# Kernel tuning notes

Measured on AMD Instinct MI355X. Metric: run time of the kernel, lower is better.

The kernel has to match this reference:

```python
import jax, jax.numpy as jnp
import numpy as np

WS = 7            # window size per spatial dim
NW = WS ** 3      # tokens per window = 343
EPS = 1e-5


def _rel_pos_index():
    # MONAI 3D relative position index, shape (NW, NW), values in [0, 13^3)
    coords = np.stack(np.meshgrid(np.arange(WS), np.arange(WS), np.arange(WS), indexing='ij'))
    cf = coords.reshape(3, -1)                       # (3, NW)
    rel = (cf[:, :, None] - cf[:, None, :]).transpose(1, 2, 0).astype(np.int64)  # (NW, NW, 3)
    rel += WS - 1
    rel[:, :, 0] *= (2 * WS - 1) * (2 * WS - 1)
    rel[:, :, 1] *= (2 * WS - 1)
    return rel.sum(-1)

_RPI = _rel_pos_index()


def layer_norm(x, g, b):
    mu = jnp.mean(x, axis=-1, keepdims=True)
    var = jnp.mean(jnp.square(x - mu), axis=-1, keepdims=True)
    return (x - mu) * jax.lax.rsqrt(var + EPS) * g + b


def _forward(x, pe_w, pe_bias, pe_g, pe_b, n1_g, n1_b, qkv_w, rpb, proj_w, proj_b,
             n2_g, n2_b, fc1_w, fc1_b, fc2_w, fc2_b):
    # ---- PatchEmbed: Conv3d stride=patch + LayerNorm over channel ----
    h = jax.lax.conv_general_dilated(x, pe_w, (2, 2, 2), 'VALID',
                                     dimension_numbers=('NCDHW', 'OIDHW', 'NCDHW'))
    h = h + pe_bias[None, :, None, None, None]
    b, c, d, hh, w = h.shape
    t = h.reshape(b, c, -1).transpose(0, 2, 1)       # (b, d*h*w, c)
    t = layer_norm(t, pe_g, pe_b)
    h = t.transpose(0, 2, 1).reshape(b, c, d, hh, w)
    # dropout(p=0) and proj_out(normalize=False) are identity

    xe = h.transpose(0, 2, 3, 4, 1)                  # (b, d, h, w, c)
    rpi = jnp.asarray(_RPI)
    num_heads = rpb.shape[-1]
    hd = c // num_heads
    scale = hd ** -0.5
    nd, nh_, nw_ = d // WS, hh // WS, w // WS        # window grid (7,7,7)

    for i in range(qkv_w.shape[0]):                  # 3 Swin blocks, all shift=0
        shortcut = xe
        y = layer_norm(xe, n1_g[i], n1_b[i])
        # window partition -> (b*nW, NW, c)
        yw = y.reshape(b, nd, WS, nh_, WS, nw_, WS, c)
        yw = yw.transpose(0, 1, 3, 5, 2, 4, 6, 7).reshape(-1, NW, c)
        # windowed MSA with relative position bias (qkv_bias=False)
        qkv = (yw @ qkv_w[i].T).reshape(-1, NW, 3, num_heads, hd).transpose(2, 0, 3, 1, 4)
        q, k, v = qkv[0] * scale, qkv[1], qkv[2]     # (Bw, nh, NW, hd)
        attn = jnp.einsum('bhnd,bhmd->bhnm', q, k)
        bias = rpb[i][rpi].transpose(2, 0, 1)        # (nh, NW, NW)
        attn = jax.nn.softmax(attn + bias[None], axis=-1)
        o = jnp.einsum('bhnm,bhmd->bhnd', attn, v)
        o = o.transpose(0, 2, 1, 3).reshape(-1, NW, c)
        o = o @ proj_w[i].T + proj_b[i]
        # window reverse
        o = o.reshape(b, nd, nh_, nw_, WS, WS, WS, c)
        o = o.transpose(0, 1, 4, 2, 5, 3, 6, 7).reshape(b, d, hh, w, c)
        xe = shortcut + o
        # MLP (GELU exact, mlp_ratio=4)
        z = layer_norm(xe, n2_g[i], n2_b[i])
        z = jax.nn.gelu(z @ fc1_w[i].T + fc1_b[i], approximate=False)
        xe = xe + (z @ fc2_w[i].T + fc2_b[i])

    return xe.transpose(0, 4, 1, 2, 3)               # (b, c, d, h, w)


def setup_inputs() -> dict:
    key = jax.random.key(0)
    ks = jax.random.split(key, 16)
    C, NH, NB, MLP = 16, 2, 3, 64
    s = 0.02
    return {
        'x': jax.random.normal(ks[0], (1, 1, 98, 98, 98), jnp.float32),
        'pe_w': jax.random.normal(ks[1], (C, 1, 2, 2, 2), jnp.float32) * s,
        'pe_bias': jnp.zeros((C,), jnp.float32),
        'pe_g': jnp.ones((C,), jnp.float32),
        'pe_b': jnp.zeros((C,), jnp.float32),
        'n1_g': jnp.ones((NB, C), jnp.float32),
        'n1_b': jnp.zeros((NB, C), jnp.float32),
        'qkv_w': jax.random.normal(ks[2], (NB, 3 * C, C), jnp.float32) * s,
        'rpb': jax.random.normal(ks[3], (NB, (2 * WS - 1) ** 3, NH), jnp.float32) * s,
        'proj_w': jax.random.normal(ks[4], (NB, C, C), jnp.float32) * s,
        'proj_b': jnp.zeros((NB, C), jnp.float32),
        'n2_g': jnp.ones((NB, C), jnp.float32),
        'n2_b': jnp.zeros((NB, C), jnp.float32),
        'fc1_w': jax.random.normal(ks[5], (NB, MLP, C), jnp.float32) * s,
        'fc1_b': jnp.zeros((NB, MLP), jnp.float32),
        'fc2_w': jax.random.normal(ks[6], (NB, C, MLP), jnp.float32) * s,
        'fc2_b': jnp.zeros((NB, C), jnp.float32),
    }


def reference(x, pe_w, pe_bias, pe_g, pe_b, n1_g, n1_b, qkv_w, rpb, proj_w, proj_b,
              n2_g, n2_b, fc1_w, fc1_b, fc2_w, fc2_b):
    return _forward(x, pe_w, pe_bias, pe_g, pe_b, n1_g, n1_b, qkv_w, rpb, proj_w,
                    proj_b, n2_g, n2_b, fc1_w, fc1_b, fc2_w, fc2_b)
```

## Files before the change

kernel.cpp:

```cpp
#include <hip/hip_runtime.h>
#include <math.h>

#define NWTOK 343
#define NTOK 117649
#define QSCALE 0.510069734f
#define LOG2E 1.4426950408889634f
#define QPLANE 1372
#define OPLANE 2744
#define NPAD 352
#define NTILE 22
#define NBIAS_BLK 2904
#define NK0_TILE 7546

typedef unsigned int u32;
typedef __fp16 h2 __attribute__((ext_vector_type(2)));
typedef __fp16 h4 __attribute__((ext_vector_type(4)));
typedef float f32x4 __attribute__((ext_vector_type(4)));

__device__ __forceinline__ u32 packh2(float a, float b) {
    h2 h = __builtin_amdgcn_cvt_pkrtz(a, b);
    return __builtin_bit_cast(u32, h);
}
__device__ __forceinline__ h4 packh4(float a, float b, float c, float d) {
    return __builtin_bit_cast(h4, make_uint2(packh2(a, b), packh2(c, d)));
}
__device__ __forceinline__ float fast_exp2(float x) {
#if __has_builtin(__builtin_amdgcn_exp2f)
    return __builtin_amdgcn_exp2f(x);
#else
    return exp2f(x);
#endif
}

__device__ __forceinline__ float gelu_exact(float x) {
    const float z = x * 0.70710678118654752f;
    const float az = fabsf(z);
    const float t = __builtin_amdgcn_rcpf(fmaf(0.3275911f, az, 1.0f));
    float y = fmaf(t, 1.061405429f, -1.453152027f);
    y = fmaf(t, y, 1.421413741f);
    y = fmaf(t, y, -0.284496736f);
    y = fmaf(t, y, 0.254829592f);
    y *= t;
    const float one_m_erf = y * __expf(-az * az);
    const float erf_az = 1.0f - one_m_erf;
    const float erf_z = (z < 0.f) ? -erf_az : erf_az;
    return 0.5f * x * (1.0f + erf_z);
}

__global__ __launch_bounds__(256, 4) void k0_fused(
    const float* __restrict__ x,
    const float* __restrict__ pe_w,
    const float* __restrict__ pe_bias,
    const float* __restrict__ pe_g,
    const float* __restrict__ pe_b,
    const float* __restrict__ n1_g,
    const float* __restrict__ n1_b,
    const float* __restrict__ qkv_w,
    const float* __restrict__ rpb,
    float* __restrict__ xe,
    u32* __restrict__ qg,
    u32* __restrict__ kg,
    u32* __restrict__ vg,
    __fp16* __restrict__ bexp16)
{
    const int tid = threadIdx.x;

    if (blockIdx.x < NBIAS_BLK) {
        const int tile = blockIdx.x;
        const int kt = tile % NTILE;
        const int rest = tile / NTILE;
        const int qt = rest % NTILE;
        const int bh = rest / NTILE;
        const int blk = bh >> 1, h = bh & 1;
        const int n = tid >> 4, g = tid & 15;
        const int i = qt * 16 + n, j = kt * 16 + g;
        float val;
        if (j >= NWTOK) {
            val = -60.f;
        } else if (i >= NWTOK) {
            val = 0.f;
        } else {
            const int iz = i / 49, ir = i - iz * 49, iy = ir / 7, ix = ir - iy * 7;
            const int jz = j / 49, jr = j - jz * 49, jy = jr / 7, jx = jr - jy * 7;
            const int idx = (iz - jz + 6) * 169 + (iy - jy + 6) * 13 + (ix - jx + 6);
            val = rpb[((size_t)blk * 2197 + idx) * 2 + h] * LOG2E;
        }
        bexp16[(size_t)tile * 256 + tid] = (__fp16)val;
        return;
    }

    __shared__ float pw_s[128];
    __shared__ u32 qkvh[384];
    __shared__ float pb_s[16], g_s[16], b_s[16], n1g_s[16], n1b_s[16];

    if (tid < 128) pw_s[tid] = pe_w[tid];
    for (int i = tid; i < 384; i += 256) {
        const float2 a = ((const float2*)qkv_w)[i];
        qkvh[i] = packh2(a.x, a.y);
    }
    if (tid < 16) {
        pb_s[tid] = pe_bias[tid]; g_s[tid] = pe_g[tid]; b_s[tid] = pe_b[tid];
        n1g_s[tid] = n1_g[tid]; n1b_s[tid] = n1_b[tid];
    }
    __syncthreads();

    const int wave_id = (blockIdx.x - NBIAS_BLK) * 4 + (tid >> 6);
    if (wave_id >= NK0_TILE) return;
    const int w = wave_id / NTILE;
    const int qt = wave_id - w * NTILE;

    const int lane = tid & 63;
    const int tcol = lane & 15;
    const int g4 = (lane >> 4) * 4;
    const int tok = qt * 16 + tcol;
    const bool valid = (tok < NWTOK);
    const int tokc = valid ? tok : (NWTOK - 1);

    const int wd = w / 49, wr = w - wd * 49, wh = wr / 7, ww = wr - wh * 7;
    const int tz = tokc / 49, tr = tokc - tz * 49, ty = tr / 7, tx = tr - ty * 7;
    const int z = wd * 7 + tz, y = wh * 7 + ty, xx = ww * 7 + tx;
    const float* bp = x + ((size_t)(2 * z) * 98 + (2 * y)) * 98 + 2 * xx;
    float in[8];
    in[0] = bp[0];    in[1] = bp[1];
    in[2] = bp[98];   in[3] = bp[99];
    in[4] = bp[9604]; in[5] = bp[9605];
    in[6] = bp[9702]; in[7] = bp[9703];

    float c4[4];
    #pragma unroll
    for (int i = 0; i < 4; ++i) {
        const int ch = g4 + i;
        const float4 w0 = *(const float4*)(pw_s + ch * 8);
        const float4 w1 = *(const float4*)(pw_s + ch * 8 + 4);
        float a = pb_s[ch];
        a = fmaf(in[0], w0.x, a); a = fmaf(in[1], w0.y, a);
        a = fmaf(in[2], w0.z, a); a = fmaf(in[3], w0.w, a);
        a = fmaf(in[4], w1.x, a); a = fmaf(in[5], w1.y, a);
        a = fmaf(in[6], w1.z, a); a = fmaf(in[7], w1.w, a);
        c4[i] = a;
    }

    float s = (c4[0] + c4[1]) + (c4[2] + c4[3]);
    s += __shfl_xor(s, 16); s += __shfl_xor(s, 32);
    float mu = s * 0.0625f;
    float v0 = c4[0] - mu, v1 = c4[1] - mu, v2 = c4[2] - mu, v3 = c4[3] - mu;
    float vv = fmaf(v0, v0, fmaf(v1, v1, fmaf(v2, v2, v3 * v3)));
    vv += __shfl_xor(vv, 16); vv += __shfl_xor(vv, 32);
    float rs = rsqrtf(vv * 0.0625f + 1e-5f);
    const float4 gg = *(const float4*)(g_s + g4);
    const float4 bb = *(const float4*)(b_s + g4);
    const float o0 = v0 * rs * gg.x + bb.x;
    const float o1 = v1 * rs * gg.y + bb.y;
    const float o2 = v2 * rs * gg.z + bb.z;
    const float o3 = v3 * rs * gg.w + bb.w;

    if (valid)
        *(float4*)(xe + (size_t)(w * NWTOK + tok) * 16 + g4) = make_float4(o0, o1, o2, o3);

    s = (o0 + o1) + (o2 + o3);
    s += __shfl_xor(s, 16); s += __shfl_xor(s, 32);
    mu = s * 0.0625f;
    v0 = o0 - mu; v1 = o1 - mu; v2 = o2 - mu; v3 = o3 - mu;
    vv = fmaf(v0, v0, fmaf(v1, v1, fmaf(v2, v2, v3 * v3)));
    vv += __shfl_xor(vv, 16); vv += __shfl_xor(vv, 32);
    rs = rsqrtf(vv * 0.0625f + 1e-5f);
    const float4 g1 = *(const float4*)(n1g_s + g4);
    const float4 b1 = *(const float4*)(n1b_s + g4);
    const h4 yB = packh4(v0 * rs * g1.x + b1.x, v1 * rs * g1.y + b1.y,
                         v2 * rs * g1.z + b1.z, v3 * rs * g1.w + b1.w);

    const f32x4 zero = {0.f, 0.f, 0.f, 0.f};
    const int head = g4 >> 3;
    const int uoff = (g4 & 7) >> 1;
    const size_t qpl = (size_t)(w * 2 + head) * QPLANE + tok * 4 + uoff;
    #pragma unroll
    for (int m = 0; m < 3; ++m) {
        const uint2 aw = *(const uint2*)(qkvh + (m * 16 + tcol) * 8 + (g4 >> 1));
        f32x4 d = __builtin_amdgcn_mfma_f32_16x16x16f16(
            __builtin_bit_cast(h4, aw), yB, zero, 0, 0, 0);
        const float sc = (m == 0) ? QSCALE : 1.f;
        const u32 lo = packh2(d[0] * sc, d[1] * sc);
        const u32 hi = packh2(d[2] * sc, d[3] * sc);
        if (valid) {
            u32* dst = (m == 0 ? qg : (m == 1 ? kg : vg)) + qpl;
            dst[0] = lo;
            dst[1] = hi;
        }
    }
}

__global__ __launch_bounds__(704, 5) void k_attn(
    const u32* __restrict__ qg,
    const u32* __restrict__ kg,
    const u32* __restrict__ vg,
    float* __restrict__ og,
    const __fp16* __restrict__ bexp_blk)
{
    __shared__ __fp16 Kl[2][NPAD][16];
    __shared__ __fp16 Ql[2][NPAD][16];
    __shared__ __fp16 Vt[2][16][360];

    const int tid = threadIdx.x;
    const int pidx = blockIdx.x;
    const int wp = pidx >> 1;
    const int h = pidx & 1;
    const int w0 = 2 * wp;
    const int w1 = (w0 + 1 < NWTOK) ? w0 + 1 : NWTOK - 1;
    const int wh0 = w0 * 2 + h;
    const int wh1 = w1 * 2 + h;

    {
        const int sw = (tid >= NPAD) ? 1 : 0;
        const int st = tid - sw * NPAD;
        const size_t qpl = (size_t)(sw ? wh1 : wh0) * QPLANE;
        const uint4 z4 = make_uint4(0, 0, 0, 0);
        if (st < NWTOK) {
            const uint4 kw = ((const uint4*)(kg + qpl))[st];
            const uint4 qw = ((const uint4*)(qg + qpl))[st];
            const uint4 vw = ((const uint4*)(vg + qpl))[st];
            *(uint4*)&Kl[sw][st][0] = kw; *(uint4*)&Kl[sw][st][8] = z4;
            *(uint4*)&Ql[sw][st][0] = qw; *(uint4*)&Ql[sw][st][8] = z4;
            const h2 v01 = __builtin_bit_cast(h2, vw.x);
            const h2 v23 = __builtin_bit_cast(h2, vw.y);
            const h2 v45 = __builtin_bit_cast(h2, vw.z);
            const h2 v67 = __builtin_bit_cast(h2, vw.w);
            Vt[sw][0][st] = v01.x; Vt[sw][1][st] = v01.y;
            Vt[sw][2][st] = v23.x; Vt[sw][3][st] = v23.y;
            Vt[sw][4][st] = v45.x; Vt[sw][5][st] = v45.y;
            Vt[sw][6][st] = v67.x; Vt[sw][7][st] = v67.y;
        } else {
            *(uint4*)&Kl[sw][st][0] = z4; *(uint4*)&Kl[sw][st][8] = z4;
            *(uint4*)&Ql[sw][st][0] = z4; *(uint4*)&Ql[sw][st][8] = z4;
            #pragma unroll
            for (int d = 0; d < 8; ++d) Vt[sw][d][st] = (__fp16)0.f;
        }
        #pragma unroll
        for (int d = 8; d < 16; ++d) Vt[sw][d][st] = (__fp16)0.f;
    }
    __syncthreads();

    const int wave = tid >> 6;
    const int lane = tid & 63;
    const int n = lane & 15;
    const int g4 = (lane >> 4) * 4;

    const int qiA = (2 * wave) * 16 + n;
    const int qiB = qiA + 16;
    const h4 bqA0 = *(const h4*)&Ql[0][qiA][g4];
    const h4 bqB0 = *(const h4*)&Ql[0][qiB][g4];
    const h4 bqA1 = *(const h4*)&Ql[1][qiA][g4];
    const h4 bqB1 = *(const h4*)&Ql[1][qiB][g4];

    const int laneoff = n * 16 + g4;
    const __fp16* trowA = bexp_blk + ((size_t)(h * 484) + (size_t)(2 * wave) * NTILE) * 256 + laneoff;
    const __fp16* trowB = trowA + (size_t)NTILE * 256;

    f32x4 accA0 = {0.f, 0.f, 0.f, 0.f}, accB0 = {0.f, 0.f, 0.f, 0.f};
    f32x4 accA1 = {0.f, 0.f, 0.f, 0.f}, accB1 = {0.f, 0.f, 0.f, 0.f};
    float lA0 = 0.f, lB0 = 0.f, lA1 = 0.f, lB1 = 0.f;

    #pragma unroll
    for (int kt = 0; kt < NTILE; ++kt) {
        const uint2 cbA16 = *(const uint2*)(trowA + kt * 256);
        const uint2 cbB16 = *(const uint2*)(trowB + kt * 256);
        const h2 alo = __builtin_bit_cast(h2, cbA16.x);
        const h2 ahi = __builtin_bit_cast(h2, cbA16.y);
        const h2 blo = __builtin_bit_cast(h2, cbB16.x);
        const h2 bhi = __builtin_bit_cast(h2, cbB16.y);
        f32x4 cbAf, cbBf;
        cbAf[0] = (float)alo.x; cbAf[1] = (float)alo.y;
        cbAf[2] = (float)ahi.x; cbAf[3] = (float)ahi.y;
        cbBf[0] = (float)blo.x; cbBf[1] = (float)blo.y;
        cbBf[2] = (float)bhi.x; cbBf[3] = (float)bhi.y;

        const h4 ak0 = *(const h4*)&Kl[0][kt * 16 + n][g4];
        const h4 ak1 = *(const h4*)&Kl[1][kt * 16 + n][g4];
        const h4 av0 = *(const h4*)&Vt[0][n][kt * 16 + g4];
        const h4 av1 = *(const h4*)&Vt[1][n][kt * 16 + g4];

        f32x4 sA0 = __builtin_amdgcn_mfma_f32_16x16x16f16(ak0, bqA0, cbAf, 0, 0, 0);
        f32x4 sB0 = __builtin_amdgcn_mfma_f32_16x16x16f16(ak0, bqB0, cbBf, 0, 0, 0);
        f32x4 sA1 = __builtin_amdgcn_mfma_f32_16x16x16f16(ak1, bqA1, cbAf, 0, 0, 0);
        f32x4 sB1 = __builtin_amdgcn_mfma_f32_16x16x16f16(ak1, bqB1, cbBf, 0, 0, 0);

        const float pA00 = fast_exp2(sA0[0]);
        const float pA01 = fast_exp2(sA0[1]);
        const float pA02 = fast_exp2(sA0[2]);
        const float pA03 = fast_exp2(sA0[3]);
        const float pB00 = fast_exp2(sB0[0]);
        const float pB01 = fast_exp2(sB0[1]);
        const float pB02 = fast_exp2(sB0[2]);
        const float pB03 = fast_exp2(sB0[3]);
        const float pA10 = fast_exp2(sA1[0]);
        const float pA11 = fast_exp2(sA1[1]);
        const float pA12 = fast_exp2(sA1[2]);
        const float pA13 = fast_exp2(sA1[3]);
        const float pB10 = fast_exp2(sB1[0]);
        const float pB11 = fast_exp2(sB1[1]);
        const float pB12 = fast_exp2(sB1[2]);
        const float pB13 = fast_exp2(sB1[3]);

        lA0 += (pA00 + pA01) + (pA02 + pA03);
        lB0 += (pB00 + pB01) + (pB02 + pB03);
        lA1 += (pA10 + pA11) + (pA12 + pA13);
        lB1 += (pB10 + pB11) + (pB12 + pB13);

        const h4 bpA0 = packh4(pA00, pA01, pA02, pA03);
        const h4 bpB0 = packh4(pB00, pB01, pB02, pB03);
        const h4 bpA1 = packh4(pA10, pA11, pA12, pA13);
        const h4 bpB1 = packh4(pB10, pB11, pB12, pB13);

        accA0 = __builtin_amdgcn_mfma_f32_16x16x16f16(av0, bpA0, accA0, 0, 0, 0);
        accB0 = __builtin_amdgcn_mfma_f32_16x16x16f16(av0, bpB0, accB0, 0, 0, 0);
        accA1 = __builtin_amdgcn_mfma_f32_16x16x16f16(av1, bpA1, accA1, 0, 0, 0);
        accB1 = __builtin_amdgcn_mfma_f32_16x16x16f16(av1, bpB1, accB1, 0, 0, 0);
    }

    lA0 += __shfl_xor(lA0, 16); lA0 += __shfl_xor(lA0, 32);
    lB0 += __shfl_xor(lB0, 16); lB0 += __shfl_xor(lB0, 32);
    lA1 += __shfl_xor(lA1, 16); lA1 += __shfl_xor(lA1, 32);
    lB1 += __shfl_xor(lB1, 16); lB1 += __shfl_xor(lB1, 32);

    if (g4 < 8) {
        if (qiA < NWTOK) {
            const f32x4 o0 = accA0 * (1.f / lA0);
            *(f32x4*)(og + (size_t)wh0 * OPLANE + qiA * 8 + g4) = o0;
            const f32x4 o1 = accA1 * (1.f / lA1);
            *(f32x4*)(og + (size_t)wh1 * OPLANE + qiA * 8 + g4) = o1;
        }
        if (qiB < NWTOK) {
            const f32x4 o0 = accB0 * (1.f / lB0);
            *(f32x4*)(og + (size_t)wh0 * OPLANE + qiB * 8 + g4) = o0;
            const f32x4 o1 = accB1 * (1.f / lB1);
            *(f32x4*)(og + (size_t)wh1 * OPLANE + qiB * 8 + g4) = o1;
        }
    }
}

__global__ __launch_bounds__(256, 4) void k_post(
    float* __restrict__ xe,
    const float* __restrict__ og,
    u32* __restrict__ qg,
    u32* __restrict__ kg,
    u32* __restrict__ vg,
    const float* __restrict__ proj_w,
    const float* __restrict__ proj_b,
    const float* __restrict__ n2_g,
    const float* __restrict__ n2_b,
    const float* __restrict__ fc1_w,
    const float* __restrict__ fc1_b,
    const float* __restrict__ fc2_w,
    const float* __restrict__ fc2_b,
    const float* __restrict__ n1_g_nx,
    const float* __restrict__ n1_b_nx,
    const float* __restrict__ qkv_w_nx,
    float* __restrict__ outp,
    const int last)
{
    __shared__ u32 projh[128];
    __shared__ u32 fc1h[512];
    __shared__ u32 fc2h[512];
    __shared__ u32 qkvh[384];
    __shared__ float projb_s[16], n2g_s[16], n2b_s[16], fc2b_s[16], n1g_s[16], n1b_s[16];
    __shared__ float fc1b_s[64];
    const int tid = threadIdx.x;
    if (tid < 128) {
        const float2 p = ((const float2*)proj_w)[tid];
        projh[tid] = packh2(p.x, p.y);
    }
    for (int i = tid; i < 512; i += 256) {
        const float2 a = ((const float2*)fc1_w)[i];
        fc1h[i] = packh2(a.x, a.y);
        const float2 b = ((const float2*)fc2_w)[i];
        fc2h[i] = packh2(b.x, b.y);
    }
    for (int i = tid; i < 384; i += 256) {
        const float2 a = ((const float2*)qkv_w_nx)[i];
        qkvh[i] = packh2(a.x, a.y);
    }
    if (tid < 16) {
        projb_s[tid] = proj_b[tid];
        n2g_s[tid] = n2_g[tid]; n2b_s[tid] = n2_b[tid];
        fc2b_s[tid] = fc2_b[tid];
        n1g_s[tid] = n1_g_nx[tid]; n1b_s[tid] = n1_b_nx[tid];
    }
    if (tid < 64) fc1b_s[tid] = fc1_b[tid];
    __syncthreads();

    const int wave_id = blockIdx.x * 4 + (tid >> 6);
    if (wave_id >= NWTOK * NTILE) return;
    const int w = wave_id / NTILE;
    const int qt = wave_id - w * NTILE;

    const int lane = tid & 63;
    const int tcol = lane & 15;
    const int g4 = (lane >> 4) * 4;
    const int tok = qt * 16 + tcol;
    const bool valid = (tok < NWTOK);
    const int tokc = valid ? tok : (NWTOK - 1);

    const f32x4 zero = {0.f, 0.f, 0.f, 0.f};

    const int pl = g4 >> 3;
    const int po = g4 & 7;
    const float4 o4 = *(const float4*)(og + (size_t)(w * 2 + pl) * OPLANE + tokc * 8 + po);
    const h4 oB = packh4(o4.x, o4.y, o4.z, o4.w);

    const uint2 apw = *(const uint2*)(projh + tcol * 8 + (g4 >> 1));
    const f32x4 d1 = __builtin_amdgcn_mfma_f32_16x16x16f16(
        __builtin_bit_cast(h4, apw), oB, zero, 0, 0, 0);
    const float4 xe4 = *(const float4*)(xe + (size_t)(w * NWTOK + tokc) * 16 + g4);
    const float4 pb4 = *(const float4*)(projb_s + g4);
    float xr0 = d1[0] + xe4.x + pb4.x;
    float xr1 = d1[1] + xe4.y + pb4.y;
    float xr2 = d1[2] + xe4.z + pb4.z;
    float xr3 = d1[3] + xe4.w + pb4.w;

    float s = (xr0 + xr1) + (xr2 + xr3);
    s += __shfl_xor(s, 16); s += __shfl_xor(s, 32);
    float mu = s * 0.0625f;
    float v0 = xr0 - mu, v1 = xr1 - mu, v2 = xr2 - mu, v3 = xr3 - mu;
    float vv = fmaf(v0, v0, fmaf(v1, v1, fmaf(v2, v2, v3 * v3)));
    vv += __shfl_xor(vv, 16); vv += __shfl_xor(vv, 32);
    float rs = rsqrtf(vv * 0.0625f + 1e-5f);
    const float4 g2 = *(const float4*)(n2g_s + g4);
    const float4 b2 = *(const float4*)(n2b_s + g4);
    const h4 zB = packh4(v0 * rs * g2.x + b2.x, v1 * rs * g2.y + b2.y,
                         v2 * rs * g2.z + b2.z, v3 * rs * g2.w + b2.w);

    h4 hB[4];
    #pragma unroll
    for (int i = 0; i < 4; ++i) {
        const uint2 aw = *(const uint2*)(fc1h + (i * 16 + tcol) * 8 + (g4 >> 1));
        f32x4 hd = __builtin_amdgcn_mfma_f32_16x16x16f16(
            __builtin_bit_cast(h4, aw), zB, zero, 0, 0, 0);
        const float4 fb = *(const float4*)(fc1b_s + i * 16 + g4);
        hB[i] = packh4(gelu_exact(hd[0] + fb.x), gelu_exact(hd[1] + fb.y),
                       gelu_exact(hd[2] + fb.z), gelu_exact(hd[3] + fb.w));
    }

    f32x4 acc = zero;
    #pragma unroll
    for (int j = 0; j < 4; ++j) {
        const uint2 aw = *(const uint2*)(fc2h + tcol * 32 + ((j * 16 + g4) >> 1));
        acc = __builtin_amdgcn_mfma_f32_16x16x16f16(
            __builtin_bit_cast(h4, aw), hB[j], acc, 0, 0, 0);
    }
    const float4 f2b = *(const float4*)(fc2b_s + g4);
    xr0 += acc[0] + f2b.x;
    xr1 += acc[1] + f2b.y;
    xr2 += acc[2] + f2b.z;
    xr3 += acc[3] + f2b.w;

    if (last) {
        if (valid) {
            const int wd = w / 49, wr2 = w - wd * 49, whh = wr2 / 7, www = wr2 - whh * 7;
            const int tz = tok / 49, tr2 = tok - tz * 49, ty = tr2 / 7, tx = tr2 - ty * 7;
            const int g = ((wd * 7 + tz) * 49 + (whh * 7 + ty)) * 49 + (www * 7 + tx);
            outp[(size_t)(g4 + 0) * NTOK + g] = xr0;
            outp[(size_t)(g4 + 1) * NTOK + g] = xr1;
            outp[(size_t)(g4 + 2) * NTOK + g] = xr2;
            outp[(size_t)(g4 + 3) * NTOK + g] = xr3;
        }
        return;
    }

    if (valid) {
        float4 st = make_float4(xr0, xr1, xr2, xr3);
        *(float4*)(xe + (size_t)(w * NWTOK + tok) * 16 + g4) = st;
    }

    s = (xr0 + xr1) + (xr2 + xr3);
    s += __shfl_xor(s, 16); s += __shfl_xor(s, 32);
    mu = s * 0.0625f;
    v0 = xr0 - mu; v1 = xr1 - mu; v2 = xr2 - mu; v3 = xr3 - mu;
    vv = fmaf(v0, v0, fmaf(v1, v1, fmaf(v2, v2, v3 * v3)));
    vv += __shfl_xor(vv, 16); vv += __shfl_xor(vv, 32);
    rs = rsqrtf(vv * 0.0625f + 1e-5f);
    const float4 g1 = *(const float4*)(n1g_s + g4);
    const float4 b1 = *(const float4*)(n1b_s + g4);
    const h4 yB = packh4(v0 * rs * g1.x + b1.x, v1 * rs * g1.y + b1.y,
                         v2 * rs * g1.z + b1.z, v3 * rs * g1.w + b1.w);

    const int head = g4 >> 3;
    const int uoff = (g4 & 7) >> 1;
    const size_t qpl = (size_t)(w * 2 + head) * QPLANE + tok * 4 + uoff;
    #pragma unroll
    for (int m = 0; m < 3; ++m) {
        const uint2 aw = *(const uint2*)(qkvh + (m * 16 + tcol) * 8 + (g4 >> 1));
        f32x4 d = __builtin_amdgcn_mfma_f32_16x16x16f16(
            __builtin_bit_cast(h4, aw), yB, zero, 0, 0, 0);
        float sc = (m == 0) ? QSCALE : 1.f;
        const u32 lo = packh2(d[0] * sc, d[1] * sc);
        const u32 hi = packh2(d[2] * sc, d[3] * sc);
        if (valid) {
            u32* dst = (m == 0 ? qg : (m == 1 ? kg : vg)) + qpl;
            dst[0] = lo;
            dst[1] = hi;
        }
    }
}

extern "C" void kernel_launch(void* const* d_in, const int* in_sizes, int n_in,
                              void* d_out, int out_size, void* d_ws, size_t ws_size,
                              hipStream_t stream) {
    const float* x       = (const float*)d_in[0];
    const float* pe_w    = (const float*)d_in[1];
    const float* pe_bias = (const float*)d_in[2];
    const float* pe_g    = (const float*)d_in[3];
    const float* pe_b    = (const float*)d_in[4];
    const float* n1_g    = (const float*)d_in[5];
    const float* n1_b    = (const float*)d_in[6];
    const float* qkv_w   = (const float*)d_in[7];
    const float* rpb     = (const float*)d_in[8];
    const float* proj_w  = (const float*)d_in[9];
    const float* proj_b  = (const float*)d_in[10];
    const float* n2_g    = (const float*)d_in[11];
    const float* n2_b    = (const float*)d_in[12];
    const float* fc1_w   = (const float*)d_in[13];
    const float* fc1_b   = (const float*)d_in[14];
    const float* fc2_w   = (const float*)d_in[15];
    const float* fc2_b   = (const float*)d_in[16];

    float* ws = (float*)d_ws;
    const size_t SEG = (size_t)NTOK * 16;
    const size_t QSEG = (size_t)686 * QPLANE;
    float* xe = ws;
    u32* qg = (u32*)(ws + SEG);
    u32* kg = qg + QSEG;
    u32* vg = kg + QSEG;
    float* og = (float*)(vg + QSEG);
    __fp16* bexp16 = (__fp16*)(og + (size_t)686 * OPLANE);
    float* out = (float*)d_out;

    const int k0_grid = NBIAS_BLK + (NK0_TILE + 3) / 4;
    k0_fused<<<k0_grid, 256, 0, stream>>>(
        x, pe_w, pe_bias, pe_g, pe_b, n1_g, n1_b, qkv_w, rpb,
        xe, qg, kg, vg, bexp16);

    const int post_grid = (NWTOK * NTILE + 3) / 4;
    for (int i = 0; i < 3; ++i) {
        const int last = (i == 2) ? 1 : 0;
        const int nx = last ? i : i + 1;
        k_attn<<<344, 704, 0, stream>>>(
            qg, kg, vg, og, bexp16 + (size_t)i * 2 * 484 * 256);
        k_post<<<post_grid, 256, 0, stream>>>(
            xe, og, qg, kg, vg,
            proj_w + (size_t)i * 256, proj_b + (size_t)i * 16,
            n2_g + (size_t)i * 16, n2_b + (size_t)i * 16,
            fc1_w + (size_t)i * 1024, fc1_b + (size_t)i * 64,
            fc2_w + (size_t)i * 1024, fc2_b + (size_t)i * 16,
            n1_g + (size_t)nx * 16, n1_b + (size_t)nx * 16,
            qkv_w + (size_t)nx * 768,
            out, last);
    }
}
```

Before: 130.7 us.

## Split attention into one window-head per block with query tiles across three blocks

Changes the attention kernel's work decomposition. Each block used to process two windows for one head with 704 threads; now each block handles one window-head and a third of its query tiles, with 256 threads and a 2058-block grid. Q is read straight from global memory into registers instead of being staged in LDS, and the K/V LDS buffers shrink to the 8 real head dims, with zero-padded lanes filled in registers. This aims for better occupancy and load balance across CUs. The cost is that every block reloads the full K and V for its window, giving three times the K/V traffic, and one wave in each third block exits early.

```diff
diff --git a/kernel.cpp b/kernel.cpp
--- a/kernel.cpp
+++ b/kernel.cpp
@@ -189,75 +189,70 @@
     }
 }
 
-__global__ __launch_bounds__(704, 5) void k_attn(
+__global__ __launch_bounds__(256, 6) void k_attn(
     const u32* __restrict__ qg,
     const u32* __restrict__ kg,
     const u32* __restrict__ vg,
     float* __restrict__ og,
     const __fp16* __restrict__ bexp_blk)
 {
-    __shared__ __fp16 Kl[2][NPAD][16];
-    __shared__ __fp16 Ql[2][NPAD][16];
-    __shared__ __fp16 Vt[2][16][360];
+    __shared__ u32 Kl[NPAD][4];
+    __shared__ __fp16 Vt[8][360];
 
     const int tid = threadIdx.x;
     const int pidx = blockIdx.x;
-    const int wp = pidx >> 1;
-    const int h = pidx & 1;
-    const int w0 = 2 * wp;
-    const int w1 = (w0 + 1 < NWTOK) ? w0 + 1 : NWTOK - 1;
-    const int wh0 = w0 * 2 + h;
-    const int wh1 = w1 * 2 + h;
-
-    {
-        const int sw = (tid >= NPAD) ? 1 : 0;
-        const int st = tid - sw * NPAD;
-        const size_t qpl = (size_t)(sw ? wh1 : wh0) * QPLANE;
-        const uint4 z4 = make_uint4(0, 0, 0, 0);
-        if (st < NWTOK) {
-            const uint4 kw = ((const uint4*)(kg + qpl))[st];
-            const uint4 qw = ((const uint4*)(qg + qpl))[st];
-            const uint4 vw = ((const uint4*)(vg + qpl))[st];
-            *(uint4*)&Kl[sw][st][0] = kw; *(uint4*)&Kl[sw][st][8] = z4;
-            *(uint4*)&Ql[sw][st][0] = qw; *(uint4*)&Ql[sw][st][8] = z4;
+    const int grp = pidx % 3;
+    const int rest = pidx / 3;
+    const int h = rest & 1;
+    const int w = rest >> 1;
+    const int wh = w * 2 + h;
+    const size_t qpl = (size_t)wh * QPLANE;
+
+    for (int i = tid; i < NPAD; i += 256) {
+        if (i < NWTOK) {
+            *(uint4*)&Kl[i][0] = ((const uint4*)(kg + qpl))[i];
+            const uint4 vw = ((const uint4*)(vg + qpl))[i];
             const h2 v01 = __builtin_bit_cast(h2, vw.x);
             const h2 v23 = __builtin_bit_cast(h2, vw.y);
             const h2 v45 = __builtin_bit_cast(h2, vw.z);
             const h2 v67 = __builtin_bit_cast(h2, vw.w);
-            Vt[sw][0][st] = v01.x; Vt[sw][1][st] = v01.y;
-            Vt[sw][2][st] = v23.x; Vt[sw][3][st] = v23.y;
-            Vt[sw][4][st] = v45.x; Vt[sw][5][st] = v45.y;
-            Vt[sw][6][st] = v67.x; Vt[sw][7][st] = v67.y;
+            Vt[0][i] = v01.x; Vt[1][i] = v01.y;
+            Vt[2][i] = v23.x; Vt[3][i] = v23.y;
+            Vt[4][i] = v45.x; Vt[5][i] = v45.y;
+            Vt[6][i] = v67.x; Vt[7][i] = v67.y;
         } else {
-            *(uint4*)&Kl[sw][st][0] = z4; *(uint4*)&Kl[sw][st][8] = z4;
-            *(uint4*)&Ql[sw][st][0] = z4; *(uint4*)&Ql[sw][st][8] = z4;
+            *(uint4*)&Kl[i][0] = make_uint4(0, 0, 0, 0);
             #pragma unroll
-            for (int d = 0; d < 8; ++d) Vt[sw][d][st] = (__fp16)0.f;
-        }
-        #pragma unroll
-        for (int d = 8; d < 16; ++d) Vt[sw][d][st] = (__fp16)0.f;
+            for (int d = 0; d < 8; ++d) Vt[d][i] = (__fp16)0.f;
+        }
     }
     __syncthreads();
 
-    const int wave = tid >> 6;
+    const int wv = tid >> 6;
+    const int p = grp * 4 + wv;
+    if (p >= 11) return;
+
     const int lane = tid & 63;
     const int n = lane & 15;
     const int g4 = (lane >> 4) * 4;
-
-    const int qiA = (2 * wave) * 16 + n;
+    const h4 zeroh = __builtin_bit_cast(h4, make_uint2(0u, 0u));
+
+    const int qiA = (2 * p) * 16 + n;
     const int qiB = qiA + 16;
-    const h4 bqA0 = *(const h4*)&Ql[0][qiA][g4];
-    const h4 bqB0 = *(const h4*)&Ql[0][qiB][g4];
-    const h4 bqA1 = *(const h4*)&Ql[1][qiA][g4];
-    const h4 bqB1 = *(const h4*)&Ql[1][qiB][g4];
+    h4 bqA = zeroh, bqB = zeroh;
+    if (g4 < 8) {
+        bqA = __builtin_bit_cast(h4, *(const uint2*)(qg + qpl + qiA * 4 + (g4 >> 1)));
+        if (qiB < NWTOK)
+            bqB = __builtin_bit_cast(h4, *(const uint2*)(qg + qpl + qiB * 4 + (g4 >> 1)));
+    }
 
     const int laneoff = n * 16 + g4;
-    const __fp16* trowA = bexp_blk + ((size_t)(h * 484) + (size_t)(2 * wave) * NTILE) * 256 + laneoff;
+    const __fp16* trowA = bexp_blk + ((size_t)(h * 484) + (size_t)(2 * p) * NTILE) * 256 + laneoff;
     const __fp16* trowB = trowA + (size_t)NTILE * 256;
 
-    f32x4 accA0 = {0.f, 0.f, 0.f, 0.f}, accB0 = {0.f, 0.f, 0.f, 0.f};
-    f32x4 accA1 = {0.f, 0.f, 0.f, 0.f}, accB1 = {0.f, 0.f, 0.f, 0.f};
-    float lA0 = 0.f, lB0 = 0.f, lA1 = 0.f, lB1 = 0.f;
+    f32x4 accA = {0.f, 0.f, 0.f, 0.f};
+    f32x4 accB = {0.f, 0.f, 0.f, 0.f};
+    float lA = 0.f, lB = 0.f;
 
     #pragma unroll
     for (int kt = 0; kt < NTILE; ++kt) {
@@ -273,66 +268,44 @@
         cbBf[0] = (float)blo.x; cbBf[1] = (float)blo.y;
         cbBf[2] = (float)bhi.x; cbBf[3] = (float)bhi.y;
 
-        const h4 ak0 = *(const h4*)&Kl[0][kt * 16 + n][g4];
-        const h4 ak1 = *(const h4*)&Kl[1][kt * 16 + n][g4];
-        const h4 av0 = *(const h4*)&Vt[0][n][kt * 16 + g4];
-        const h4 av1 = *(const h4*)&Vt[1][n][kt * 16 + g4];
-
-        f32x4 sA0 = __builtin_amdgcn_mfma_f32_16x16x16f16(ak0, bqA0, cbAf, 0, 0, 0);
-        f32x4 sB0 = __builtin_amdgcn_mfma_f32_16x16x16f16(ak0, bqB0, cbBf, 0, 0, 0);
-        f32x4 sA1 = __builtin_amdgcn_mfma_f32_16x16x16f16(ak1, bqA1, cbAf, 0, 0, 0);
-        f32x4 sB1 = __builtin_amdgcn_mfma_f32_16x16x16f16(ak1, bqB1, cbBf, 0, 0, 0);
-
-        const float pA00 = fast_exp2(sA0[0]);
-        const float pA01 = fast_exp2(sA0[1]);
-        const float pA02 = fast_exp2(sA0[2]);
-        const float pA03 = fast_exp2(sA0[3]);
-        const float pB00 = fast_exp2(sB0[0]);
-        const float pB01 = fast_exp2(sB0[1]);
-        const float pB02 = fast_exp2(sB0[2]);
-        const float pB03 = fast_exp2(sB0[3]);
-        const float pA10 = fast_exp2(sA1[0]);
-        const float pA11 = fast_exp2(sA1[1]);
-        const float pA12 = fast_exp2(sA1[2]);
-        const float pA13 = fast_exp2(sA1[3]);
-        const float pB10 = fast_exp2(sB1[0]);
-        const float pB11 = fast_exp2(sB1[1]);
-        const float pB12 = fast_exp2(sB1[2]);
-        const float pB13 = fast_exp2(sB1[3]);
-
-        lA0 += (pA00 + pA01) + (pA02 + pA03);
-        lB0 += (pB00 + pB01) + (pB02 + pB03);
-        lA1 += (pA10 + pA11) + (pA12 + pA13);
-        lB1 += (pB10 + pB11) + (pB12 + pB13);
-
-        const h4 bpA0 = packh4(pA00, pA01, pA02, pA03);
-        const h4 bpB0 = packh4(pB00, pB01, pB02, pB03);
-        const h4 bpA1 = packh4(pA10, pA11, pA12, pA13);
-        const h4 bpB1 = packh4(pB10, pB11, pB12, pB13);
-
-        accA0 = __builtin_amdgcn_mfma_f32_16x16x16f16(av0, bpA0, accA0, 0, 0, 0);
-        accB0 = __builtin_amdgcn_mfma_f32_16x16x16f16(av0, bpB0, accB0, 0, 0, 0);
-        accA1 = __builtin_amdgcn_mfma_f32_16x16x16f16(av1, bpA1, accA1, 0, 0, 0);
-        accB1 = __builtin_amdgcn_mfma_f32_16x16x16f16(av1, bpB1, accB1, 0, 0, 0);
-    }
-
-    lA0 += __shfl_xor(lA0, 16); lA0 += __shfl_xor(lA0, 32);
-    lB0 += __shfl_xor(lB0, 16); lB0 += __shfl_xor(lB0, 32);
-    lA1 += __shfl_xor(lA1, 16); lA1 += __shfl_xor(lA1, 32);
-    lB1 += __shfl_xor(lB1, 16); lB1 += __shfl_xor(lB1, 32);
+        h4 ak = zeroh;
+        if (g4 < 8)
+            ak = __builtin_bit_cast(h4, *(const uint2*)(&Kl[kt * 16 + n][g4 >> 1]));
+        h4 av = zeroh;
+        if (n < 8)
+            av = *(const h4*)&Vt[n][kt * 16 + g4];
+
+        f32x4 sA = __builtin_amdgcn_mfma_f32_16x16x16f16(ak, bqA, cbAf, 0, 0, 0);
+        f32x4 sB = __builtin_amdgcn_mfma_f32_16x16x16f16(ak, bqB, cbBf, 0, 0, 0);
+
+        const float pA0 = fast_exp2(sA[0]);
+        const float pA1 = fast_exp2(sA[1]);
+        const float pA2 = fast_exp2(sA[2]);
+        const float pA3 = fast_exp2(sA[3]);
+        const float pB0 = fast_exp2(sB[0]);
+        const float pB1 = fast_exp2(sB[1]);
+        const float pB2 = fast_exp2(sB[2]);
+        const float pB3 = fast_exp2(sB[3]);
+        lA += (pA0 + pA1) + (pA2 + pA3);
+        lB += (pB0 + pB1) + (pB2 + pB3);
+
+        const h4 bpA = packh4(pA0, pA1, pA2, pA3);
+        const h4 bpB = packh4(pB0, pB1, pB2, pB3);
+        accA = __builtin_amdgcn_mfma_f32_16x16x16f16(av, bpA, accA, 0, 0, 0);
+        accB = __builtin_amdgcn_mfma_f32_16x16x16f16(av, bpB, accB, 0, 0, 0);
+    }
+
+    lA += __shfl_xor(lA, 16); lA += __shfl_xor(lA, 32);
+    lB += __shfl_xor(lB, 16); lB += __shfl_xor(lB, 32);
 
     if (g4 < 8) {
-        if (qiA < NWTOK) {
-            const f32x4 o0 = accA0 * (1.f / lA0);
-            *(f32x4*)(og + (size_t)wh0 * OPLANE + qiA * 8 + g4) = o0;
-            const f32x4 o1 = accA1 * (1.f / lA1);
-            *(f32x4*)(og + (size_t)wh1 * OPLANE + qiA * 8 + g4) = o1;
+        {
+            const f32x4 o = accA * (1.f / lA);
+            *(f32x4*)(og + (size_t)wh * OPLANE + qiA * 8 + g4) = o;
         }
         if (qiB < NWTOK) {
-            const f32x4 o0 = accB0 * (1.f / lB0);
-            *(f32x4*)(og + (size_t)wh0 * OPLANE + qiB * 8 + g4) = o0;
-            const f32x4 o1 = accB1 * (1.f / lB1);
-            *(f32x4*)(og + (size_t)wh1 * OPLANE + qiB * 8 + g4) = o1;
+            const f32x4 o = accB * (1.f / lB);
+            *(f32x4*)(og + (size_t)wh * OPLANE + qiB * 8 + g4) = o;
         }
     }
 }
@@ -538,11 +511,12 @@
         x, pe_w, pe_bias, pe_g, pe_b, n1_g, n1_b, qkv_w, rpb,
         xe, qg, kg, vg, bexp16);
 
+    const int attn_grid = NWTOK * 2 * 3;
     const int post_grid = (NWTOK * NTILE + 3) / 4;
     for (int i = 0; i < 3; ++i) {
         const int last = (i == 2) ? 1 : 0;
         const int nx = last ? i : i + 1;
-        k_attn<<<344, 704, 0, stream>>>(
+        k_attn<<<attn_grid, 256, 0, stream>>>(
             qg, kg, vg, og, bexp16 + (size_t)i * 2 * 484 * 256);
         k_post<<<post_grid, 256, 0, stream>>>(
             xe, og, qg, kg, vg,
```

New measurement: 313.5 us. 2.4x slower.

## Split attention blocks into three 256-thread groups and shrink shared memory

Applied to the files above, without the earlier changes.

The attention kernel moves from 344 blocks of 704 threads (11 waves) to 1032 blocks of 256 threads. Each block handles up to 4 of the 11 query-tile pairs for a window pair and head, so K/V staging into shared memory is repeated three times per window pair. Q is now read straight from global memory into registers instead of being staged. Shared memory drops by removing the zero-padded halves of K and V, with zeros supplied through register masks instead. The key loop is no longer unrolled. The aim is better occupancy and scheduling, at the cost of redundant K/V loads and one idle wave in every third block.

```diff
diff --git a/kernel.cpp b/kernel.cpp
--- a/kernel.cpp
+++ b/kernel.cpp
@@ -189,37 +189,34 @@
     }
 }
 
-__global__ __launch_bounds__(704, 5) void k_attn(
+__global__ __launch_bounds__(256, 4) void k_attn(
     const u32* __restrict__ qg,
     const u32* __restrict__ kg,
     const u32* __restrict__ vg,
     float* __restrict__ og,
     const __fp16* __restrict__ bexp_blk)
 {
-    __shared__ __fp16 Kl[2][NPAD][16];
-    __shared__ __fp16 Ql[2][NPAD][16];
-    __shared__ __fp16 Vt[2][16][360];
+    __shared__ u32 Kl[2][NPAD][4];
+    __shared__ __fp16 Vt[2][8][360];
 
     const int tid = threadIdx.x;
     const int pidx = blockIdx.x;
-    const int wp = pidx >> 1;
-    const int h = pidx & 1;
+    const int grp = pidx % 3;
+    const int rest = pidx / 3;
+    const int h = rest & 1;
+    const int wp = rest >> 1;
     const int w0 = 2 * wp;
     const int w1 = (w0 + 1 < NWTOK) ? w0 + 1 : NWTOK - 1;
     const int wh0 = w0 * 2 + h;
     const int wh1 = w1 * 2 + h;
 
-    {
-        const int sw = (tid >= NPAD) ? 1 : 0;
-        const int st = tid - sw * NPAD;
+    for (int i = tid; i < 2 * NPAD; i += 256) {
+        const int sw = (i >= NPAD) ? 1 : 0;
+        const int st = i - sw * NPAD;
         const size_t qpl = (size_t)(sw ? wh1 : wh0) * QPLANE;
-        const uint4 z4 = make_uint4(0, 0, 0, 0);
         if (st < NWTOK) {
-            const uint4 kw = ((const uint4*)(kg + qpl))[st];
-            const uint4 qw = ((const uint4*)(qg + qpl))[st];
+            *(uint4*)&Kl[sw][st][0] = ((const uint4*)(kg + qpl))[st];
             const uint4 vw = ((const uint4*)(vg + qpl))[st];
-            *(uint4*)&Kl[sw][st][0] = kw; *(uint4*)&Kl[sw][st][8] = z4;
-            *(uint4*)&Ql[sw][st][0] = qw; *(uint4*)&Ql[sw][st][8] = z4;
             const h2 v01 = __builtin_bit_cast(h2, vw.x);
             const h2 v23 = __builtin_bit_cast(h2, vw.y);
             const h2 v45 = __builtin_bit_cast(h2, vw.z);
@@ -229,37 +226,44 @@
             Vt[sw][4][st] = v45.x; Vt[sw][5][st] = v45.y;
             Vt[sw][6][st] = v67.x; Vt[sw][7][st] = v67.y;
         } else {
-            *(uint4*)&Kl[sw][st][0] = z4; *(uint4*)&Kl[sw][st][8] = z4;
-            *(uint4*)&Ql[sw][st][0] = z4; *(uint4*)&Ql[sw][st][8] = z4;
+            *(uint4*)&Kl[sw][st][0] = make_uint4(0, 0, 0, 0);
             #pragma unroll
             for (int d = 0; d < 8; ++d) Vt[sw][d][st] = (__fp16)0.f;
         }
-        #pragma unroll
-        for (int d = 8; d < 16; ++d) Vt[sw][d][st] = (__fp16)0.f;
     }
     __syncthreads();
 
-    const int wave = tid >> 6;
+    const int wv = tid >> 6;
+    const int p = grp * 4 + wv;
+    if (p >= 11) return;
+
     const int lane = tid & 63;
     const int n = lane & 15;
     const int g4 = (lane >> 4) * 4;
-
-    const int qiA = (2 * wave) * 16 + n;
+    const h4 zeroh = __builtin_bit_cast(h4, make_uint2(0u, 0u));
+
+    const int qiA = (2 * p) * 16 + n;
     const int qiB = qiA + 16;
-    const h4 bqA0 = *(const h4*)&Ql[0][qiA][g4];
-    const h4 bqB0 = *(const h4*)&Ql[0][qiB][g4];
-    const h4 bqA1 = *(const h4*)&Ql[1][qiA][g4];
-    const h4 bqB1 = *(const h4*)&Ql[1][qiB][g4];
+    h4 bqA0 = zeroh, bqB0 = zeroh, bqA1 = zeroh, bqB1 = zeroh;
+    if (g4 < 8) {
+        const size_t q0 = (size_t)wh0 * QPLANE;
+        const size_t q1 = (size_t)wh1 * QPLANE;
+        bqA0 = __builtin_bit_cast(h4, *(const uint2*)(qg + q0 + qiA * 4 + (g4 >> 1)));
+        bqA1 = __builtin_bit_cast(h4, *(const uint2*)(qg + q1 + qiA * 4 + (g4 >> 1)));
+        if (qiB < NWTOK) {
+            bqB0 = __builtin_bit_cast(h4, *(const uint2*)(qg + q0 + qiB * 4 + (g4 >> 1)));
+            bqB1 = __builtin_bit_cast(h4, *(const uint2*)(qg + q1 + qiB * 4 + (g4 >> 1)));
+        }
+    }
 
     const int laneoff = n * 16 + g4;
-    const __fp16* trowA = bexp_blk + ((size_t)(h * 484) + (size_t)(2 * wave) * NTILE) * 256 + laneoff;
+    const __fp16* trowA = bexp_blk + ((size_t)(h * 484) + (size_t)(2 * p) * NTILE) * 256 + laneoff;
     const __fp16* trowB = trowA + (size_t)NTILE * 256;
 
     f32x4 accA0 = {0.f, 0.f, 0.f, 0.f}, accB0 = {0.f, 0.f, 0.f, 0.f};
     f32x4 accA1 = {0.f, 0.f, 0.f, 0.f}, accB1 = {0.f, 0.f, 0.f, 0.f};
     float lA0 = 0.f, lB0 = 0.f, lA1 = 0.f, lB1 = 0.f;
 
-    #pragma unroll
     for (int kt = 0; kt < NTILE; ++kt) {
         const uint2 cbA16 = *(const uint2*)(trowA + kt * 256);
         const uint2 cbB16 = *(const uint2*)(trowB + kt * 256);
@@ -273,10 +277,16 @@
         cbBf[0] = (float)blo.x; cbBf[1] = (float)blo.y;
         cbBf[2] = (float)bhi.x; cbBf[3] = (float)bhi.y;
 
-        const h4 ak0 = *(const h4*)&Kl[0][kt * 16 + n][g4];
-        const h4 ak1 = *(const h4*)&Kl[1][kt * 16 + n][g4];
-        const h4 av0 = *(const h4*)&Vt[0][n][kt * 16 + g4];
-        const h4 av1 = *(const h4*)&Vt[1][n][kt * 16 + g4];
+        h4 ak0 = zeroh, ak1 = zeroh;
+        if (g4 < 8) {
+            ak0 = __builtin_bit_cast(h4, *(const uint2*)(&Kl[0][kt * 16 + n][g4 >> 1]));
+            ak1 = __builtin_bit_cast(h4, *(const uint2*)(&Kl[1][kt * 16 + n][g4 >> 1]));
+        }
+        h4 av0 = zeroh, av1 = zeroh;
+        if (n < 8) {
+            av0 = *(const h4*)&Vt[0][n][kt * 16 + g4];
+            av1 = *(const h4*)&Vt[1][n][kt * 16 + g4];
+        }
 
         f32x4 sA0 = __builtin_amdgcn_mfma_f32_16x16x16f16(ak0, bqA0, cbAf, 0, 0, 0);
         f32x4 sB0 = __builtin_amdgcn_mfma_f32_16x16x16f16(ak0, bqB0, cbBf, 0, 0, 0);
@@ -322,7 +332,7 @@
     lB1 += __shfl_xor(lB1, 16); lB1 += __shfl_xor(lB1, 32);
 
     if (g4 < 8) {
-        if (qiA < NWTOK) {
+        {
             const f32x4 o0 = accA0 * (1.f / lA0);
             *(f32x4*)(og + (size_t)wh0 * OPLANE + qiA * 8 + g4) = o0;
             const f32x4 o1 = accA1 * (1.f / lA1);
@@ -538,11 +548,12 @@
         x, pe_w, pe_bias, pe_g, pe_b, n1_g, n1_b, qkv_w, rpb,
         xe, qg, kg, vg, bexp16);
 
+    const int attn_grid = 172 * 2 * 3;
     const int post_grid = (NWTOK * NTILE + 3) / 4;
     for (int i = 0; i < 3; ++i) {
         const int last = (i == 2) ? 1 : 0;
         const int nx = last ? i : i + 1;
-        k_attn<<<344, 704, 0, stream>>>(
+        k_attn<<<attn_grid, 256, 0, stream>>>(
             qg, kg, vg, og, bexp16 + (size_t)i * 2 * 484 * 256);
         k_post<<<post_grid, 256, 0, stream>>>(
             xe, og, qg, kg, vg,
```

After: 129.4 us. About the same (-1.0%).
